# Kernel tuning notes

Hardware: AMD Instinct MI355X
Metric: run time of the kernel (lower is better)

The kernel has to match this reference:

```python
import jax, jax.numpy as jnp
import numpy as np
from jax import lax

B, DIM, H, W = 2, 96, 256, 256
HEADS, WIN = 4, 8
HID = int(DIM * 2.66)  # ffn hidden_features = 255


def setup_inputs() -> dict:
    key = jax.random.key(0)
    ks = jax.random.split(key, 8)
    s = 0.02
    return {
        "x": jax.random.normal(ks[0], (B, DIM, H, W), jnp.float32),
        "to_hidden_w": jax.random.normal(ks[1], (6 * DIM, DIM), jnp.float32) * s,
        "to_hidden_dw_w": jax.random.normal(ks[2], (6 * DIM, 1, 3, 3), jnp.float32) * s,
        "project_out_w": jax.random.normal(ks[3], (DIM, 2 * DIM), jnp.float32) * s,
        "temperature": jnp.ones((HEADS, 1, 1, 1), jnp.float32),
        "norm1_w": jnp.ones((DIM,), jnp.float32),
        "norm2_w": jnp.ones((DIM,), jnp.float32),
        "ffn_in_w": jax.random.normal(ks[4], (2 * HID, DIM), jnp.float32) * s,
        "ffn_dw_w": jax.random.normal(ks[5], (2 * HID, 1, 3, 3), jnp.float32) * s,
        "ffn_out_w": jax.random.normal(ks[6], (DIM, HID), jnp.float32) * s,
    }


def _ln_biasfree(x, w):
    # BiasFree_LayerNorm over channel dim (torch var over last dim of b,(hw),c)
    v = jnp.var(x, axis=1, keepdims=True)
    return x / jnp.sqrt(v + 1e-5) * w[None, :, None, None]


def _conv1x1(x, w):
    return jnp.einsum('bchw,oc->bohw', x, w)


def _dwconv3(x, w):
    return lax.conv_general_dilated(x, w, (1, 1), [(1, 1), (1, 1)],
                                    feature_group_count=x.shape[1],
                                    dimension_numbers=('NCHW', 'OIHW', 'NCHW'))


def _to_patch(t):
    # b (head c) (h p1) (w p2) -> b head (h w) c (p1 p2)
    b, hc, hh, ww = t.shape
    c, h, w = hc // HEADS, hh // WIN, ww // WIN
    t = t.reshape(b, HEADS, c, h, WIN, w, WIN)
    t = t.transpose(0, 1, 3, 5, 2, 4, 6)
    return t.reshape(b, HEADS, h * w, c, WIN * WIN)


def _from_patch(t, hh, ww):
    # b head (h w) c (p1 p2) -> b (head c) (h p1) (w p2)
    b, hd, hw, c, pp = t.shape
    h, w = hh // WIN, ww // WIN
    t = t.reshape(b, hd, h, w, c, WIN, WIN)
    t = t.transpose(0, 1, 4, 2, 5, 3, 6)
    return t.reshape(b, hd * c, hh, ww)


def _attn(x, to_hidden_w, to_hidden_dw_w, project_out_w, temperature):
    hh, ww = x.shape[-2:]
    hidden = _dwconv3(_conv1x1(x, to_hidden_w), to_hidden_dw_w)
    q, k, v = jnp.split(hidden, 3, axis=1)
    qf = jnp.fft.rfft(_to_patch(q), axis=-1)
    kf = jnp.fft.rfft(_to_patch(k), axis=-1)
    vf = jnp.fft.rfft(_to_patch(v), axis=-1)
    attn = jnp.einsum('bhpcf,bhpcg->bhpfg', qf, kf) * temperature[None]
    nrm = jnp.sqrt(jnp.sum(jnp.abs(attn) ** 2, axis=-1, keepdims=True))  # complex last-dim vector norm
    attn = attn / nrm
    out = jnp.einsum('bhpfg,bhpcg->bhpcf', attn, vf)  # (attn @ vf^T)^T -> b head p c f
    out = jnp.fft.irfft(out, n=WIN * WIN, axis=-1)
    return _conv1x1(_from_patch(out, hh, ww), project_out_w)


def _ffn(x, w_in, w_dw, w_out):
    t = _dwconv3(_conv1x1(x, w_in), w_dw)
    x1, x2 = jnp.split(t, 2, axis=1)
    return _conv1x1(jax.nn.gelu(x1, approximate=False) * x2, w_out)


def reference(x, to_hidden_w, to_hidden_dw_w, project_out_w, temperature,
              norm1_w, norm2_w, ffn_in_w, ffn_dw_w, ffn_out_w):
    x = x + _attn(_ln_biasfree(x, norm1_w), to_hidden_w, to_hidden_dw_w,
                  project_out_w, temperature)
    x = x + _ffn(_ln_biasfree(x, norm2_w), ffn_in_w, ffn_dw_w, ffn_out_w)
    return x
```

## Files before the change

kernel.cpp:

```cpp
#include <hip/hip_runtime.h>
#include <hip/hip_bf16.h>
#include <math.h>

#define HW 65536
typedef __hip_bfloat16 bf16;
typedef __attribute__((ext_vector_type(8))) short short8;
typedef __attribute__((ext_vector_type(4))) float float4v;

__device__ __forceinline__ float bf2f(bf16 h) { return __bfloat162float(h); }
__device__ __forceinline__ bf16  f2bf(float f) { return __float2bfloat16(f); }
__device__ __forceinline__ float bflo(unsigned u){ return __uint_as_float(u << 16); }
__device__ __forceinline__ float bfhi(unsigned u){ return __uint_as_float(u & 0xffff0000u); }
__device__ __forceinline__ float bits2f(unsigned short u){ return __uint_as_float(((unsigned)u) << 16); }
__device__ __forceinline__ unsigned short f2bfbits(float f){
  bf16 h = __float2bfloat16(f);
  unsigned short u; __builtin_memcpy(&u, &h, 2); return u;
}
__device__ __forceinline__ bool io_is_f32(const unsigned short* tflag) {
  return tflag[0] == 0;
}
#define C64 0.09817477042468103f

__global__ __launch_bounds__(256) void convert_params(
    const void* p1, const void* p2, const void* p3, const void* p4,
    const void* p5, const void* p6, const void* p7, const void* p8,
    const void* p9, bf16* dst) {
  int i = blockIdx.x * 256 + threadIdx.x;
  if (i >= 157042) return;
  bool f32 = io_is_f32((const unsigned short*)p4);
  #define RD(src, j) (f32 ? ((const float*)(src))[j] : bits2f(((const unsigned short*)(src))[j]))
  float v;
  if      (i < 55296)  { v = RD(p1, i) * RD(p5, i % 96); }
  else if (i < 60480)  { v = RD(p2, i - 55296); }
  else if (i < 78912)  { v = RD(p3, i - 60480); }
  else if (i < 78916)  { v = RD(p4, i - 78912); }
  else if (i < 127876) { int j = i - 78916;  v = RD(p7, j) * RD(p6, j % 96); }
  else if (i < 132466) { v = RD(p8, i - 127876); }
  else {
    int j = i - 132466;
    int o = j >> 8, c = j & 255;
    v = (c < 255) ? RD(p9, o*255 + c) : 0.f;
  }
  #undef RD
  dst[i] = f2bf(v);
}

template<bool EXT>
__global__ __launch_bounds__(256) void ln_pre(const void* __restrict__ in,
                                              bf16* __restrict__ out, size_t eoff,
                                              const unsigned short* __restrict__ tflag) {
  int t = blockIdx.x * 256 + threadIdx.x;
  int p = t >> 1;
  int half = t & 1;
  const bool f32 = EXT && io_is_f32(tflag);
  float v[48];
  float s = 0.f, s2 = 0.f;
  #pragma unroll
  for (int j = 0; j < 48; ++j) {
    size_t off = (size_t)(half*48 + j) * HW + p;
    float xv = EXT ? (f32 ? ((const float*)in)[eoff + off]
                          : bits2f(((const unsigned short*)in)[eoff + off]))
                   : bits2f(((const unsigned short*)in)[off]);
    v[j] = xv; s += xv; s2 += xv*xv;
  }
  s  += __shfl_xor(s, 1);
  s2 += __shfl_xor(s2, 1);
  float mean = s * (1.f/96.f);
  float var  = s2 * (1.f/96.f) - mean*mean;
  float inv  = rsqrtf(fmaxf(var, 0.f) + 1e-5f);
  unsigned short* outu = (unsigned short*)out + (size_t)p*96 + half*48;
  #pragma unroll
  for (int jb = 0; jb < 6; ++jb) {
    uint4 ov;
    ov.x = f2bfbits(v[jb*8+0]*inv) | ((unsigned)f2bfbits(v[jb*8+1]*inv) << 16);
    ov.y = f2bfbits(v[jb*8+2]*inv) | ((unsigned)f2bfbits(v[jb*8+3]*inv) << 16);
    ov.z = f2bfbits(v[jb*8+4]*inv) | ((unsigned)f2bfbits(v[jb*8+5]*inv) << 16);
    ov.w = f2bfbits(v[jb*8+6]*inv) | ((unsigned)f2bfbits(v[jb*8+7]*inv) << 16);
    *(uint4*)(outu + jb*8) = ov;
  }
}

template<int CIN, int K32, int KP, int PT, int OT, int WAVES, bool IPM, bool RES,
         bool RESEXT, bool OUTEXT, bool PERM>
__global__ __launch_bounds__(WAVES*64) void conv_mfma(
    const bf16* __restrict__ in, const bf16* __restrict__ w,
    const void* __restrict__ res,
    void* __restrict__ out, size_t eoff,
    const unsigned short* __restrict__ tflag, int cout) {
  constexpr int BT = WAVES * 64;
  constexpr int NT = PT / 16;
  constexpr int MT = OT / (16 * WAVES);
  constexpr int SOS = PT + 8;
  __shared__ __align__(16) unsigned short SH[PT*KP + OT*KP];
  unsigned short (*in_lds)[KP] = (unsigned short(*)[KP])SH;
  unsigned short (*w_lds)[KP]  = (unsigned short(*)[KP])(SH + PT*KP);
  const int tid = threadIdx.x;
  const int p0 = blockIdx.x * PT;
  const int ob = blockIdx.y * OT;
  const bool iof32 = (RESEXT || OUTEXT) ? io_is_f32(tflag) : false;
  const unsigned short* inu = (const unsigned short*)in;
  const unsigned short* wu  = (const unsigned short*)w;

  #define ROTS(r) ({ int _s = (((r) >> 3) << 3); if (_s >= K32) _s -= K32; _s; })

  if constexpr (IPM) {
    for (int i = tid; i < PT*(CIN/8); i += BT) {
      int row = i / (CIN/8), cb = (i % (CIN/8)) * 8;
      uint4 v = *(const uint4*)&inu[(size_t)(p0 + row)*CIN + cb];
      int pc = cb + ROTS(row);
      if (pc >= K32) pc -= K32;
      *(uint4*)&in_lds[row][pc] = v;
    }
  } else {
    for (int i = tid; i < CIN*(PT/8); i += BT) {
      int c = i / (PT/8), p8 = (i % (PT/8)) * 8;
      uint4 v = *(const uint4*)&inu[(size_t)c*HW + p0 + p8];
      unsigned short e[8];
      e[0] = (unsigned short)(v.x); e[1] = (unsigned short)(v.x >> 16);
      e[2] = (unsigned short)(v.y); e[3] = (unsigned short)(v.y >> 16);
      e[4] = (unsigned short)(v.z); e[5] = (unsigned short)(v.z >> 16);
      e[6] = (unsigned short)(v.w); e[7] = (unsigned short)(v.w >> 16);
      #pragma unroll
      for (int j = 0; j < 8; ++j) {
        int row = p8 + j;
        int pc = c + ROTS(row);
        if (pc >= K32) pc -= K32;
        in_lds[row][pc] = e[j];
      }
    }
  }
  for (int i = tid; i < OT*(K32/8); i += BT) {
    int ol = i / (K32/8), cb = (i % (K32/8)) * 8;
    int o = ob + ol;
    uint4 v = make_uint4(0u, 0u, 0u, 0u);
    if (o < cout) v = *(const uint4*)&wu[(size_t)o*K32 + cb];
    *(uint4*)&w_lds[ol][cb] = v;
  }
  if (K32 > CIN) {
    for (int i = tid; i < (K32 - CIN) * PT; i += BT) {
      int row = i % PT, lc = CIN + i / PT;
      int pc = lc + ROTS(row);
      if (pc >= K32) pc -= K32;
      in_lds[row][pc] = 0;
    }
  }
  __syncthreads();

  const int lane = tid & 63, wave = tid >> 6;
  const int col = lane & 15, quad = lane >> 4;
  float4v acc[MT][NT];
  #pragma unroll
  for (int mt = 0; mt < MT; ++mt)
    #pragma unroll
    for (int nt = 0; nt < NT; ++nt)
      acc[mt][nt] = (float4v){0.f, 0.f, 0.f, 0.f};

  #pragma unroll
  for (int ks = 0; ks < K32/32; ++ks) {
    const int kb = ks*32 + quad*8;
    short8 a[MT];
    #pragma unroll
    for (int mt = 0; mt < MT; ++mt)
      a[mt] = *(const short8*)&w_lds[(wave + WAVES*mt)*16 + col][kb];
    #pragma unroll
    for (int nt = 0; nt < NT; ++nt) {
      const int row = nt*16 + col;
      int pkb = kb + ROTS(row);
      if (pkb >= K32) pkb -= K32;
      short8 bfr = *(const short8*)&in_lds[row][pkb];
      #pragma unroll
      for (int mt = 0; mt < MT; ++mt)
        acc[mt][nt] = __builtin_amdgcn_mfma_f32_16x16x32_bf16(a[mt], bfr, acc[mt][nt], 0, 0, 0);
    }
  }
  #undef ROTS

  __syncthreads();
  unsigned short* Sout = SH;
  #pragma unroll
  for (int mt = 0; mt < MT; ++mt) {
    #pragma unroll
    for (int nt = 0; nt < NT; ++nt) {
      const int p = nt*16 + col;
      #pragma unroll
      for (int r = 0; r < 4; ++r) {
        int ol = (wave + WAVES*mt)*16 + quad*4 + r;
        Sout[ol*SOS + p] = f2bfbits(acc[mt][nt][r]);
      }
    }
  }
  __syncthreads();

  for (int j = tid; j < OT*(PT/8); j += BT) {
    int ol = j / (PT/8), seg = j % (PT/8);
    int o = ob + ol;
    if (o >= cout) continue;
    int p = seg*8;
    int nat;
    if (PERM) {
      int pg = p0 + p;
      int window = pg >> 6, e = pg & 63;
      nat = (((window >> 5)*8 + (e >> 3)) << 8) + ((window & 31) << 3);
    } else {
      nat = p0 + p;
    }
    size_t oi = (size_t)o * HW + nat;
    uint4 hv = *(const uint4*)&Sout[ol*SOS + p];
    if (!RES && !(OUTEXT)) {
      *(uint4*)((unsigned short*)out + oi) = hv;
      continue;
    }
    float f0=bflo(hv.x), f1=bfhi(hv.x), f2=bflo(hv.y), f3=bfhi(hv.y);
    float f4=bflo(hv.z), f5=bfhi(hv.z), f6=bflo(hv.w), f7=bfhi(hv.w);
    if (RES) {
      if (RESEXT && iof32) {
        const float* rp = (const float*)res + eoff + oi;
        float4 r0 = *(const float4*)rp;
        float4 r1 = *(const float4*)(rp + 4);
        f0+=r0.x; f1+=r0.y; f2+=r0.z; f3+=r0.w;
        f4+=r1.x; f5+=r1.y; f6+=r1.z; f7+=r1.w;
      } else {
        const unsigned short* rp = (const unsigned short*)res + (RESEXT ? eoff + oi : oi);
        uint4 rv = *(const uint4*)rp;
        f0+=bflo(rv.x); f1+=bfhi(rv.x); f2+=bflo(rv.y); f3+=bfhi(rv.y);
        f4+=bflo(rv.z); f5+=bfhi(rv.z); f6+=bflo(rv.w); f7+=bfhi(rv.w);
      }
    }
    if (OUTEXT && iof32) {
      float* op = (float*)out + eoff + oi;
      *(float4*)op       = make_float4(f0, f1, f2, f3);
      *(float4*)(op + 4) = make_float4(f4, f5, f6, f7);
    } else {
      uint4 ov;
      ov.x = f2bfbits(f0) | ((unsigned)f2bfbits(f1) << 16);
      ov.y = f2bfbits(f2) | ((unsigned)f2bfbits(f3) << 16);
      ov.z = f2bfbits(f4) | ((unsigned)f2bfbits(f5) << 16);
      ov.w = f2bfbits(f6) | ((unsigned)f2bfbits(f7) << 16);
      *(uint4*)((unsigned short*)out + (OUTEXT ? eoff + oi : oi)) = ov;
    }
  }
}

__device__ __forceinline__ void dw9x8(const unsigned short* __restrict__ pin,
                                      const bf16* __restrict__ w,
                                      int y, int x0, float* __restrict__ o) {
  float wv[9];
  #pragma unroll
  for (int i = 0; i < 9; ++i) wv[i] = bf2f(w[i]);
  float r[3][10];
  #pragma unroll
  for (int dy = 0; dy < 3; ++dy) {
    int yy = y + dy - 1;
    if (yy < 0 || yy > 255) {
      #pragma unroll
      for (int j = 0; j < 10; ++j) r[dy][j] = 0.f;
    } else {
      const unsigned short* row = pin + yy*256 + x0;
      uint4 q = *(const uint4*)row;
      r[dy][1] = bflo(q.x); r[dy][2] = bfhi(q.x);
      r[dy][3] = bflo(q.y); r[dy][4] = bfhi(q.y);
      r[dy][5] = bflo(q.z); r[dy][6] = bfhi(q.z);
      r[dy][7] = bflo(q.w); r[dy][8] = bfhi(q.w);
      r[dy][0] = (x0 > 0)   ? bits2f(row[-1]) : 0.f;
      r[dy][9] = (x0 < 248) ? bits2f(row[8])  : 0.f;
    }
  }
  #pragma unroll
  for (int j = 0; j < 8; ++j) {
    float s = 0.f;
    #pragma unroll
    for (int dy = 0; dy < 3; ++dy)
      #pragma unroll
      for (int dx = 0; dx < 3; ++dx)
        s += r[dy][j+dx] * wv[dy*3+dx];
    o[j] = s;
  }
}

__global__ __launch_bounds__(256) void dwconv_gate_v8(const bf16* __restrict__ in,
                                                      const bf16* __restrict__ w,
                                                      bf16* __restrict__ out) {
  int t = blockIdx.x * 256 + threadIdx.x;
  int g8 = t & 8191;
  int c  = t >> 13;
  int y  = g8 >> 5;
  int x0 = (g8 & 31) << 3;
  float d1[8], d2[8];
  dw9x8((const unsigned short*)in + ((size_t)c << 16),         w + c*9,       y, x0, d1);
  dw9x8((const unsigned short*)in + ((size_t)(c+255) << 16),   w + (c+255)*9, y, x0, d2);
  unsigned short ob[8];
  #pragma unroll
  for (int j = 0; j < 8; ++j) {
    float g = 0.5f * d1[j] * (1.f + erff(d1[j] * 0.70710678118654752f)) * d2[j];
    ob[j] = f2bfbits(g);
  }
  uint4 ov;
  ov.x = ob[0] | ((unsigned)ob[1] << 16);
  ov.y = ob[2] | ((unsigned)ob[3] << 16);
  ov.z = ob[4] | ((unsigned)ob[5] << 16);
  ov.w = ob[6] | ((unsigned)ob[7] << 16);
  *(uint4*)((unsigned short*)out + ((size_t)c << 16) + y*256 + x0) = ov;
}

__global__ __launch_bounds__(512, 8) void fft_attn_mfma(const bf16* __restrict__ hid,
                                                        const bf16* __restrict__ temp,
                                                        bf16* __restrict__ outP,
                                                        const bf16* __restrict__ wdw) {
  constexpr int RS  = 68;
  constexpr int MS  = 100;
  constexpr int RAW = 0;
  constexpr int WFo = 9792;
  constexpr int QAo = 0;
  constexpr int KB1 = 4800;
  constexpr int KB2 = 9600;
  constexpr int VAo = 14400;
  constexpr int AB1 = 0;
  constexpr int AB2 = 4800;
  constexpr int OAo = 9600;
  constexpr int WIo = 0;
  __shared__ __align__(16) unsigned short S[19200];
  __shared__ float inv_s[48];

  const int tid = threadIdx.x;
  const int lane = tid & 63, wave = tid >> 6;
  const int col = lane & 15, quad = lane >> 4;

  const int bid = blockIdx.x;
  const int sw  = ((bid & 7) << 9) | (bid >> 3);
  const int head = sw >> 10;
  const int patch = sw & 1023;
  const int y0 = (patch >> 5) * 8, x0 = (patch & 31) * 8;
  const float tscale = bf2f(temp[head]);
  const unsigned short* hidu = (const unsigned short*)hid;

  for (int i = tid; i < 1152; i += 512) {
    int tc = i >> 3, wr = i & 7;
    int chan = (tc/48)*192 + head*48 + (tc%48);
    float o[8];
    dw9x8(hidu + ((size_t)chan << 16), wdw + chan*9, y0 + wr, x0, o);
    unsigned short* d = &S[RAW + tc*RS + wr*8];
    uint2 lo = make_uint2(f2bfbits(o[0]) | ((unsigned)f2bfbits(o[1]) << 16),
                          f2bfbits(o[2]) | ((unsigned)f2bfbits(o[3]) << 16));
    uint2 hi = make_uint2(f2bfbits(o[4]) | ((unsigned)f2bfbits(o[5]) << 16),
                          f2bfbits(o[6]) | ((unsigned)f2bfbits(o[7]) << 16));
    *(uint2*)d       = lo;
    *(uint2*)(d + 4) = hi;
  }
  for (int i = tid; i < 80*64; i += 512) {
    int n = i >> 6, e = i & 63;
    float v = 0.f;
    if (n < 33)      v =  __builtin_amdgcn_cosf((float)((n*e) & 63) * 0.015625f);
    else if (n < 66) v = -__builtin_amdgcn_sinf((float)(((n-33)*e) & 63) * 0.015625f);
    S[WFo + n*RS + e] = f2bfbits(v);
  }
  __syncthreads();

  float4v dacc[6];
  #pragma unroll
  for (int k = 0; k < 6; ++k) {
    int ti = wave + 8*k;
    if (ti < 45) {
      int mt = ti/5, nt = ti%5;
      const unsigned short* arow = &S[RAW + (mt*16+col)*RS];
      const unsigned short* brow = &S[WFo + (nt*16+col)*RS];
      float4v acc = (float4v){0.f,0.f,0.f,0.f};
      #pragma unroll
      for (int ks = 0; ks < 2; ++ks)
        acc = __builtin_amdgcn_mfma_f32_16x16x32_bf16(
            *(const short8*)(arow + ks*32 + quad*8),
            *(const short8*)(brow + ks*32 + quad*8), acc, 0,0,0);
      dacc[k] = acc;
    }
  }
  __syncthreads();

  #pragma unroll
  for (int k = 0; k < 6; ++k) {
    int ti = wave + 8*k;
    if (ti < 45) {
      int mt = ti/5, nt = ti%5;
      int n = nt*16 + col;
      if (n < 66) {
        bool isre = n < 33;
        int f = isre ? n : n - 33;
        float4v acc = dacc[k];
        #pragma unroll
        for (int r = 0; r < 4; ++r) {
          int m = mt*16 + quad*4 + r;
          int t = m/48, c = m - t*48;
          unsigned short vb = f2bfbits(acc[r]);
          if (t == 0) {
            S[QAo + f*MS + (isre ? c : 48 + c)] = vb;
          } else if (t == 1) {
            if (isre) { S[KB1 + f*MS + c] = vb;  S[KB2 + f*MS + 48 + c] = vb; }
            else      { S[KB2 + f*MS + c] = vb;  S[KB1 + f*MS + 48 + c] = f2bfbits(-acc[r]); }
          } else {
            S[VAo + c*MS + (isre ? f : 48 + f)] = vb;
          }
        }
      }
    }
  }
  for (int i = tid; i < 1500; i += 512) {
    S[QAo + 3300 + i] = 0; S[KB1 + 3300 + i] = 0; S[KB2 + 3300 + i] = 0;
  }
  for (int i = tid; i < 48*30; i += 512) {
    int r = i/30, cc = i - r*30;
    S[VAo + r*MS + (cc < 15 ? 33 + cc : 66 + cc)] = 0;
  }
  __syncthreads();

  float4v qacc[3];
  #pragma unroll
  for (int k = 0; k < 3; ++k) {
    int ti = wave + 8*k;
    if (ti < 18) {
      int mat = ti/9, rem = ti - mat*9, mt = rem/3, nt = rem%3;
      const unsigned short* arow = &S[QAo + (mt*16+col)*MS];
      const unsigned short* brow = &S[(mat ? KB2 : KB1) + (nt*16+col)*MS];
      float4v acc = (float4v){0.f,0.f,0.f,0.f};
      #pragma unroll
      for (int ks = 0; ks < 3; ++ks)
        acc = __builtin_amdgcn_mfma_f32_16x16x32_bf16(
            *(const short8*)(arow + ks*32 + quad*8),
            *(const short8*)(brow + ks*32 + quad*8), acc, 0,0,0);
      qacc[k] = acc;
    }
  }
  __syncthreads();

  #pragma unroll
  for (int k = 0; k < 3; ++k) {
    int ti = wave + 8*k;
    if (ti < 18) {
      int mat = ti/9, rem = ti - mat*9, mt = rem/3, nt = rem%3;
      int g = nt*16 + col;
      #pragma unroll
      for (int r = 0; r < 4; ++r) {
        int f = mt*16 + quad*4 + r;
        float v = qacc[k][r] * tscale;
        unsigned short vb = f2bfbits(v);
        if (mat == 0) { S[AB1 + f*MS + g] = vb;  S[AB2 + f*MS + 48 + g] = vb; }
        else          { S[AB2 + f*MS + g] = vb;  S[AB1 + f*MS + 48 + g] = f2bfbits(-v); }
      }
    }
  }
  __syncthreads();

  float4v vacc[3];
  #pragma unroll
  for (int k = 0; k < 3; ++k) {
    int ti = wave + 8*k;
    if (ti < 18) {
      int mat = ti/9, rem = ti - mat*9, mt = rem/3, nt = rem%3;
      const unsigned short* arow = &S[VAo + (mt*16+col)*MS];
      const unsigned short* brow = &S[(mat ? AB2 : AB1) + (nt*16+col)*MS];
      float4v acc = (float4v){0.f,0.f,0.f,0.f};
      #pragma unroll
      for (int ks = 0; ks < 3; ++ks)
        acc = __builtin_amdgcn_mfma_f32_16x16x32_bf16(
            *(const short8*)(arow + ks*32 + quad*8),
            *(const short8*)(brow + ks*32 + quad*8), acc, 0,0,0);
      vacc[k] = acc;
    }
  }
  if (tid < 48) {
    const unsigned short* r1 = &S[AB1 + tid*MS];
    const unsigned short* r2 = &S[AB2 + tid*MS];
    float s = 0.f;
    #pragma unroll
    for (int g8 = 0; g8 < 4; ++g8) {
      uint2 a = *(const uint2*)(r1 + g8*8);
      uint2 b = *(const uint2*)(r2 + g8*8);
      float a0=bflo(a.x),a1=bfhi(a.x),a2=bflo(a.y),a3=bfhi(a.y);
      float b0=bflo(b.x),b1=bfhi(b.x),b2=bflo(b.y),b3=bfhi(b.y);
      s += a0*a0+a1*a1+a2*a2+a3*a3 + b0*b0+b1*b1+b2*b2+b3*b3;
      uint2 c = *(const uint2*)(r1 + g8*8 + 4);
      uint2 d = *(const uint2*)(r2 + g8*8 + 4);
      float c0=bflo(c.x),c1=bfhi(c.x),c2=bflo(c.y),c3=bfhi(c.y);
      float d0=bflo(d.x),d1=bfhi(d.x),d2=bflo(d.y),d3=bfhi(d.y);
      s += c0*c0+c1*c1+c2*c2+c3*c3 + d0*d0+d1*d1+d2*d2+d3*d3;
    }
    float xr = bits2f(r1[32]);
    float xi = bits2f(r2[32]);
    s += xr*xr + xi*xi;
    inv_s[tid] = 1.f / fmaxf(sqrtf(s), 1e-30f);
  }
  __syncthreads();

  #pragma unroll
  for (int k = 0; k < 3; ++k) {
    int ti = wave + 8*k;
    if (ti < 18) {
      int mat = ti/9, rem = ti - mat*9, mt = rem/3, nt = rem%3;
      int f = nt*16 + col;
      float iv = inv_s[f];
      #pragma unroll
      for (int r = 0; r < 4; ++r) {
        int c = mt*16 + quad*4 + r;
        S[OAo + c*MS + (mat ? 48 + f : f)] = f2bfbits(vacc[k][r] * iv);
      }
    }
  }
  for (int i = tid; i < 64*96; i += 512) {
    int e = i/96, k = i - e*96;
    float v = 0.f;
    if (k < 33) {
      if (k == 0)       v = 0.015625f;
      else if (k == 32) v = (e & 1) ? -0.015625f : 0.015625f;
      else              v = 0.03125f * __builtin_amdgcn_cosf((float)((k*e) & 63) * 0.015625f);
    } else if (k >= 48 && k < 81) {
      int f2 = k - 48;
      if (f2 != 0 && f2 != 32) v = -0.03125f * __builtin_amdgcn_sinf((float)((f2*e) & 63) * 0.015625f);
    }
    S[WIo + e*MS + k] = f2bfbits(v);
  }
  __syncthreads();

  {
    unsigned short* outPu = (unsigned short*)outP;
    #pragma unroll
    for (int k = 0; k < 2; ++k) {
      int ti = wave + 8*k;
      if (ti < 12) {
        int mt = ti >> 2, nt = ti & 3;
        const unsigned short* arow = &S[OAo + (mt*16+col)*MS];
        const unsigned short* brow = &S[WIo + (nt*16+col)*MS];
        float4v acc = (float4v){0.f,0.f,0.f,0.f};
        #pragma unroll
        for (int ks = 0; ks < 3; ++ks)
          acc = __builtin_amdgcn_mfma_f32_16x16x32_bf16(
              *(const short8*)(arow + ks*32 + quad*8),
              *(const short8*)(brow + ks*32 + quad*8), acc, 0,0,0);
        int e = nt*16 + col;
        #pragma unroll
        for (int r = 0; r < 4; ++r) {
          int c = mt*16 + quad*4 + r;
          outPu[(size_t)(head*48 + c)*HW + patch*64 + e] = f2bfbits(acc[r]);
        }
      }
    }
  }
}

extern "C" void kernel_launch(void* const* d_in, const int* in_sizes, int n_in,
                              void* d_out, int out_size, void* d_ws, size_t ws_size,
                              hipStream_t stream) {
  const void* x   = d_in[0];
  const unsigned short* tflag = (const unsigned short*)d_in[4];

  char* ws = (char*)d_ws;
  bf16* A   = (bf16*)(ws);
  bf16* Bb  = (bf16*)(ws + 75497472);
  bf16* X1  = (bf16*)(ws + 150994944);
  bf16* prm = (bf16*)(ws + 176160768);
  bf16* Xn  = Bb;

  bf16* w_hid     = prm + 0;
  bf16* w_hid_dw  = prm + 55296;
  bf16* w_proj    = prm + 60480;
  bf16* tempc     = prm + 78912;
  bf16* w_ffn_in  = prm + 78916;
  bf16* w_ffn_dw  = prm + 127876;
  bf16* w_ffn_out = prm + 132466;

  convert_params<<<614, 256, 0, stream>>>(d_in[1], d_in[2], d_in[3], d_in[4],
                                          d_in[5], d_in[6], d_in[7], d_in[8],
                                          d_in[9], prm);

  for (int b = 0; b < 2; ++b) {
    size_t eoff = (size_t)b * 96 * HW;
    bf16* X1b = X1 + eoff;

    ln_pre<true><<<512, 256, 0, stream>>>(x, Xn, eoff, tflag);
    conv_mfma<96,96,104,128,128, 8, true,false,false,false,false>
        <<<dim3(512,5), 512, 0, stream>>>(Xn, w_hid, nullptr, A, 0, tflag, 576);
    fft_attn_mfma<<<4096, 512, 0, stream>>>(A, tempc, Bb , w_hid_dw);
    conv_mfma<192,192,200,128,64, 4, false,true,true,false,true>
        <<<dim3(512,2), 256, 0, stream>>>(Bb, w_proj, x, X1b, eoff, tflag, 96);

    ln_pre<false><<<512, 256, 0, stream>>>(X1b, Xn, 0, tflag);
    conv_mfma<96,96,104,128,128, 8, true,false,false,false,false>
        <<<dim3(512,4), 512, 0, stream>>>(Xn, w_ffn_in, nullptr, A, 0, tflag, 510);
    dwconv_gate_v8<<<8160, 256, 0, stream>>>(A, w_ffn_dw, Bb );
    conv_mfma<255,256,264,64,64, 4, false,true,false,true,false>
        <<<dim3(1024,2), 256, 0, stream>>>(Bb, w_ffn_out, X1b, d_out, eoff, tflag, 96);
  }
}
```

Baseline: 966.0 us.

## Fuse attention output projection, residual add and second LayerNorm into one kernel

```diff
diff --git a/kernel.cpp b/kernel.cpp
--- a/kernel.cpp
+++ b/kernel.cpp
@@ -238,6 +238,151 @@
       ov.w = f2bfbits(f6) | ((unsigned)f2bfbits(f7) << 16);
       *(uint4*)((unsigned short*)out + (OUTEXT ? eoff + oi : oi)) = ov;
     }
+  }
+}
+
+__global__ __launch_bounds__(384) void proj_ln(
+    const bf16* __restrict__ in,
+    const bf16* __restrict__ w,
+    const void* __restrict__ res,
+    bf16* __restrict__ outX1,
+    bf16* __restrict__ outXn,
+    size_t eoff,
+    const unsigned short* __restrict__ tflag) {
+  constexpr int CIN = 192, K32 = 192, KP = 200, PT = 64, OT = 96, BT = 384;
+  constexpr int SOS = PT + 8;
+  __shared__ __align__(16) unsigned short SH[PT*KP + OT*KP];
+  __shared__ float invp[PT];
+  unsigned short (*in_lds)[KP] = (unsigned short(*)[KP])SH;
+  unsigned short (*w_lds)[KP]  = (unsigned short(*)[KP])(SH + PT*KP);
+  const int tid = threadIdx.x;
+  const int p0 = blockIdx.x * PT;
+  const bool iof32 = io_is_f32(tflag);
+  const unsigned short* inu = (const unsigned short*)in;
+  const unsigned short* wu  = (const unsigned short*)w;
+
+  #define ROTS(r) ({ int _s = (((r) >> 3) << 3); if (_s >= K32) _s -= K32; _s; })
+
+  for (int i = tid; i < CIN*(PT/8); i += BT) {
+    int c = i / (PT/8), p8 = (i % (PT/8)) * 8;
+    uint4 v = *(const uint4*)&inu[(size_t)c*HW + p0 + p8];
+    unsigned short e[8];
+    e[0] = (unsigned short)(v.x); e[1] = (unsigned short)(v.x >> 16);
+    e[2] = (unsigned short)(v.y); e[3] = (unsigned short)(v.y >> 16);
+    e[4] = (unsigned short)(v.z); e[5] = (unsigned short)(v.z >> 16);
+    e[6] = (unsigned short)(v.w); e[7] = (unsigned short)(v.w >> 16);
+    #pragma unroll
+    for (int j = 0; j < 8; ++j) {
+      int row = p8 + j;
+      int pc = c + ROTS(row);
+      if (pc >= K32) pc -= K32;
+      in_lds[row][pc] = e[j];
+    }
+  }
+  for (int i = tid; i < OT*(K32/8); i += BT) {
+    int ol = i / (K32/8), cb = (i % (K32/8)) * 8;
+    *(uint4*)&w_lds[ol][cb] = *(const uint4*)&wu[(size_t)ol*K32 + cb];
+  }
+  __syncthreads();
+
+  const int lane = tid & 63, wave = tid >> 6;
+  const int col = lane & 15, quad = lane >> 4;
+  float4v acc[4];
+  #pragma unroll
+  for (int nt = 0; nt < 4; ++nt) acc[nt] = (float4v){0.f,0.f,0.f,0.f};
+
+  #pragma unroll
+  for (int ks = 0; ks < K32/32; ++ks) {
+    const int kb = ks*32 + quad*8;
+    short8 a = *(const short8*)&w_lds[wave*16 + col][kb];
+    #pragma unroll
+    for (int nt = 0; nt < 4; ++nt) {
+      const int row = nt*16 + col;
+      int pkb = kb + ROTS(row);
+      if (pkb >= K32) pkb -= K32;
+      short8 bfr = *(const short8*)&in_lds[row][pkb];
+      acc[nt] = __builtin_amdgcn_mfma_f32_16x16x32_bf16(a, bfr, acc[nt], 0, 0, 0);
+    }
+  }
+  #undef ROTS
+
+  __syncthreads();
+  unsigned short* Sout = SH;
+  #pragma unroll
+  for (int nt = 0; nt < 4; ++nt) {
+    const int p = nt*16 + col;
+    #pragma unroll
+    for (int r = 0; r < 4; ++r) {
+      int ol = wave*16 + quad*4 + r;
+      Sout[ol*SOS + p] = f2bfbits(acc[nt][r]);
+    }
+  }
+  __syncthreads();
+
+  for (int j = tid; j < OT*(PT/8); j += BT) {
+    int ol = j / (PT/8), seg = j % (PT/8);
+    int p = seg*8;
+    int pg = p0 + p;
+    int window = pg >> 6, e = pg & 63;
+    int nat = (((window >> 5)*8 + (e >> 3)) << 8) + ((window & 31) << 3);
+    size_t oi = (size_t)ol * HW + nat;
+    uint4 hv = *(const uint4*)&Sout[ol*SOS + p];
+    float f0=bflo(hv.x), f1=bfhi(hv.x), f2=bflo(hv.y), f3=bfhi(hv.y);
+    float f4=bflo(hv.z), f5=bfhi(hv.z), f6=bflo(hv.w), f7=bfhi(hv.w);
+    if (iof32) {
+      const float* rp = (const float*)res + eoff + oi;
+      float4 r0 = *(const float4*)rp;
+      float4 r1 = *(const float4*)(rp + 4);
+      f0+=r0.x; f1+=r0.y; f2+=r0.z; f3+=r0.w;
+      f4+=r1.x; f5+=r1.y; f6+=r1.z; f7+=r1.w;
+    } else {
+      const unsigned short* rp = (const unsigned short*)res + eoff + oi;
+      uint4 rv = *(const uint4*)rp;
+      f0+=bflo(rv.x); f1+=bfhi(rv.x); f2+=bflo(rv.y); f3+=bfhi(rv.y);
+      f4+=bflo(rv.z); f5+=bfhi(rv.z); f6+=bflo(rv.w); f7+=bfhi(rv.w);
+    }
+    uint4 ov;
+    ov.x = f2bfbits(f0) | ((unsigned)f2bfbits(f1) << 16);
+    ov.y = f2bfbits(f2) | ((unsigned)f2bfbits(f3) << 16);
+    ov.z = f2bfbits(f4) | ((unsigned)f2bfbits(f5) << 16);
+    ov.w = f2bfbits(f6) | ((unsigned)f2bfbits(f7) << 16);
+    *(uint4*)((unsigned short*)outX1 + oi) = ov;
+    *(uint4*)&Sout[ol*SOS + p] = ov;
+  }
+  __syncthreads();
+
+  if (tid < 256) {
+    int p = tid >> 2, q = tid & 3;
+    float s = 0.f, s2 = 0.f;
+    #pragma unroll
+    for (int r = 0; r < 24; ++r) {
+      float xv = bits2f(Sout[(q*24 + r)*SOS + p]);
+      s += xv; s2 += xv*xv;
+    }
+    s  += __shfl_xor(s, 1);  s2 += __shfl_xor(s2, 1);
+    s  += __shfl_xor(s, 2);  s2 += __shfl_xor(s2, 2);
+    float mean = s * (1.f/96.f);
+    float var  = s2 * (1.f/96.f) - mean*mean;
+    if (q == 0) invp[p] = rsqrtf(fmaxf(var, 0.f) + 1e-5f);
+  }
+  __syncthreads();
+
+  for (int j = tid; j < PT*12; j += BT) {
+    int p = j / 12, cb = (j % 12) * 8;
+    int pg = p0 + p;
+    int window = pg >> 6, e = pg & 63;
+    int natp = (((window >> 5)*8 + (e >> 3)) << 8) + ((window & 31) << 3) + (e & 7);
+    float iv = invp[p];
+    unsigned short ob[8];
+    #pragma unroll
+    for (int jj = 0; jj < 8; ++jj)
+      ob[jj] = f2bfbits(bits2f(Sout[(cb + jj)*SOS + p]) * iv);
+    uint4 ov;
+    ov.x = ob[0] | ((unsigned)ob[1] << 16);
+    ov.y = ob[2] | ((unsigned)ob[3] << 16);
+    ov.z = ob[4] | ((unsigned)ob[5] << 16);
+    ov.w = ob[6] | ((unsigned)ob[7] << 16);
+    *(uint4*)((unsigned short*)outXn + (size_t)natp*96 + cb) = ov;
   }
 }
 
@@ -554,7 +699,8 @@
   bf16* Bb  = (bf16*)(ws + 75497472);
   bf16* X1  = (bf16*)(ws + 150994944);
   bf16* prm = (bf16*)(ws + 176160768);
-  bf16* Xn  = Bb;
+  bf16* Xn1 = Bb;
+  bf16* Xn2 = (bf16*)(ws + 75497472 + 50331648);
 
   bf16* w_hid     = prm + 0;
   bf16* w_hid_dw  = prm + 55296;
@@ -572,16 +718,14 @@
     size_t eoff = (size_t)b * 96 * HW;
     bf16* X1b = X1 + eoff;
 
-    ln_pre<true><<<512, 256, 0, stream>>>(x, Xn, eoff, tflag);
+    ln_pre<true><<<512, 256, 0, stream>>>(x, Xn1, eoff, tflag);
     conv_mfma<96,96,104,128,128, 8, true,false,false,false,false>
-        <<<dim3(512,5), 512, 0, stream>>>(Xn, w_hid, nullptr, A, 0, tflag, 576);
+        <<<dim3(512,5), 512, 0, stream>>>(Xn1, w_hid, nullptr, A, 0, tflag, 576);
     fft_attn_mfma<<<4096, 512, 0, stream>>>(A, tempc, Bb , w_hid_dw);
-    conv_mfma<192,192,200,128,64, 4, false,true,true,false,true>
-        <<<dim3(512,2), 256, 0, stream>>>(Bb, w_proj, x, X1b, eoff, tflag, 96);
-
-    ln_pre<false><<<512, 256, 0, stream>>>(X1b, Xn, 0, tflag);
+    proj_ln<<<1024, 384, 0, stream>>>(Bb, w_proj, x, X1b, Xn2, eoff, tflag);
+
     conv_mfma<96,96,104,128,128, 8, true,false,false,false,false>
-        <<<dim3(512,4), 512, 0, stream>>>(Xn, w_ffn_in, nullptr, A, 0, tflag, 510);
+        <<<dim3(512,4), 512, 0, stream>>>(Xn2, w_ffn_in, nullptr, A, 0, tflag, 510);
     dwconv_gate_v8<<<8160, 256, 0, stream>>>(A, w_ffn_dw, Bb );
     conv_mfma<255,256,264,64,64, 4, false,true,false,true,false>
         <<<dim3(1024,2), 256, 0, stream>>>(Bb, w_ffn_out, X1b, d_out, eoff, tflag, 96);
```

Result: slower. 988.8 us (+2.4%).
